# Performance work log

Measured on AMD Instinct MI355X. Metric: run time of the kernel, lower is better.

The kernel has to match this reference:

```python
import jax, jax.numpy as jnp
import numpy as np

EPS = 1e-06

def setup_inputs() -> dict:
    key = jax.random.key(0)
    k1, k2 = jax.random.split(key)
    x = jax.random.normal(k1, (8192, 4096), dtype=jnp.float32)
    # nn.Linear weight: [num_experts, input_dim]
    W = jax.random.normal(k2, (64, 4096), dtype=jnp.float32) * (1.0 / np.sqrt(4096.0))
    return {"x": x, "W": W}


def reference(x, W):
    # logits: [N, E]  (thin GEMM)
    logits = jnp.einsum('nd,ed->ne', x, W)
    gates = jax.nn.softmax(logits, axis=-1)
    # importance auxiliary loss: per-expert column sums, unbiased std (torch default)
    importance = gates.sum(axis=0)                      # [E]
    mean_imp = importance.mean()
    E = importance.shape[0]
    std_imp = jnp.sqrt(jnp.sum((importance - mean_imp) ** 2) / (E - 1))
    aux_loss = (std_imp / (mean_imp + EPS)) ** 2
    # top-k gates, renormalize with a second softmax
    top_k_gates, top_k_indices = jax.lax.top_k(gates, 2)  # [N, k]
    combine_weights = jax.nn.softmax(top_k_gates, axis=-1)
    return combine_weights, top_k_indices, aux_loss
```

## Files before the change

kernel.cpp:

```cpp
#include <hip/hip_runtime.h>
#include <math.h>

#define NROWS 8192
#define NK    4096
#define NE    64
#define NWV   8

typedef _Float16 f16x8 __attribute__((ext_vector_type(8)));
typedef float    f32x4 __attribute__((ext_vector_type(4)));

#define CVT8(H, L, V0, V1)                                            \
  do {                                                                \
    H[0] = (_Float16)V0.x; L[0] = (_Float16)(V0.x - (float)H[0]);     \
    H[1] = (_Float16)V0.y; L[1] = (_Float16)(V0.y - (float)H[1]);     \
    H[2] = (_Float16)V0.z; L[2] = (_Float16)(V0.z - (float)H[2]);     \
    H[3] = (_Float16)V0.w; L[3] = (_Float16)(V0.w - (float)H[3]);     \
    H[4] = (_Float16)V1.x; L[4] = (_Float16)(V1.x - (float)H[4]);     \
    H[5] = (_Float16)V1.y; L[5] = (_Float16)(V1.y - (float)H[5]);     \
    H[6] = (_Float16)V1.z; L[6] = (_Float16)(V1.z - (float)H[6]);     \
    H[7] = (_Float16)V1.w; L[7] = (_Float16)(V1.w - (float)H[7]);     \
  } while (0)

__global__ __launch_bounds__(256) void k_prep(const float* __restrict__ W,
                                              _Float16* __restrict__ Whi,
                                              _Float16* __restrict__ Wlo,
                                              float* __restrict__ imp) {
  const int idx = blockIdx.x * 256 + threadIdx.x;
  if (idx < NE) imp[idx] = 0.f;
  const int j    = idx & 7;
  const int lane = (idx >> 3) & 63;
  const int nt   = (idx >> 9) & 3;
  const int ksg  = idx >> 11;
  const int e = nt * 16 + (lane & 15);
  const int k = ksg * 32 + (lane >> 4) * 8 + j;
  const float w = W[(size_t)e * NK + k];
  const _Float16 wh = (_Float16)w;
  const _Float16 wl = (_Float16)(w - (float)wh);
  Whi[idx] = wh;
  Wlo[idx] = wl;
}

__global__ __launch_bounds__(512)
__attribute__((amdgpu_waves_per_eu(2, 2)))
void k_fused(const float* __restrict__ x,
             const _Float16* __restrict__ Whi,
             const _Float16* __restrict__ Wlo,
             float* __restrict__ out,
             float* __restrict__ imp) {
  __shared__ float plds[NWV][32][64];
  __shared__ float logit[32][64];
  __shared__ float simp[NWV][64];

  const int tid  = threadIdx.x;
  const int lane = tid & 63;
  const int wv   = __builtin_amdgcn_readfirstlane(tid >> 6);
  const int l15  = lane & 15;
  const int lhi  = lane >> 4;
  const int rbase = blockIdx.x * 32;
  const int k0    = wv * 512;

  const float* __restrict__ xp0 = x + (size_t)(rbase + l15) * NK + k0 + lhi * 8;
  const float* __restrict__ xp1 = xp0 + (size_t)16 * NK;
  const _Float16* __restrict__ whp = Whi + ((size_t)(wv * 16 * 4) * 64 + lane) * 8;
  const _Float16* __restrict__ wlp = Wlo + ((size_t)(wv * 16 * 4) * 64 + lane) * 8;

  f32x4 acc0[4], acc1[4];
#pragma unroll
  for (int nt = 0; nt < 4; ++nt) {
    acc0[nt] = (f32x4){0.f, 0.f, 0.f, 0.f};
    acc1[nt] = (f32x4){0.f, 0.f, 0.f, 0.f};
  }

  float4 ca0 = *(const float4*)(xp0);
  float4 ca1 = *(const float4*)(xp0 + 4);
  float4 cb0 = *(const float4*)(xp1);
  float4 cb1 = *(const float4*)(xp1 + 4);
  float4 na0 = *(const float4*)(xp0 + 32);
  float4 na1 = *(const float4*)(xp0 + 36);
  float4 nb0 = *(const float4*)(xp1 + 32);
  float4 nb1 = *(const float4*)(xp1 + 36);
  f16x8 whc[4], wlc[4], whn[4], wln[4];
#pragma unroll
  for (int nt = 0; nt < 4; ++nt) {
    whc[nt] = *(const f16x8*)(whp + nt * 512);
    wlc[nt] = *(const f16x8*)(wlp + nt * 512);
  }

#pragma unroll
  for (int ks = 0; ks < 16; ++ks) {
    if (ks < 15) {
      const size_t nb_ = (size_t)(ks + 1) * 2048;
#pragma unroll
      for (int nt = 0; nt < 4; ++nt) {
        whn[nt] = *(const f16x8*)(whp + nb_ + nt * 512);
        wln[nt] = *(const f16x8*)(wlp + nb_ + nt * 512);
      }
    }
    float4 pa0, pa1, pb0, pb1;
    if (ks + 2 < 16) {
      pa0 = *(const float4*)(xp0 + (ks + 2) * 32);
      pa1 = *(const float4*)(xp0 + (ks + 2) * 32 + 4);
      pb0 = *(const float4*)(xp1 + (ks + 2) * 32);
      pb1 = *(const float4*)(xp1 + (ks + 2) * 32 + 4);
    }

    f16x8 ah, al, bh, bl;
    CVT8(ah, al, ca0, ca1);
    CVT8(bh, bl, cb0, cb1);

#pragma unroll
    for (int nt = 0; nt < 4; ++nt) {
      acc0[nt] = __builtin_amdgcn_mfma_f32_16x16x32_f16(ah, whc[nt], acc0[nt], 0, 0, 0);
      acc1[nt] = __builtin_amdgcn_mfma_f32_16x16x32_f16(bh, whc[nt], acc1[nt], 0, 0, 0);
    }
#pragma unroll
    for (int nt = 0; nt < 4; ++nt) {
      acc0[nt] = __builtin_amdgcn_mfma_f32_16x16x32_f16(ah, wlc[nt], acc0[nt], 0, 0, 0);
      acc1[nt] = __builtin_amdgcn_mfma_f32_16x16x32_f16(bh, wlc[nt], acc1[nt], 0, 0, 0);
    }
#pragma unroll
    for (int nt = 0; nt < 4; ++nt) {
      acc0[nt] = __builtin_amdgcn_mfma_f32_16x16x32_f16(al, whc[nt], acc0[nt], 0, 0, 0);
      acc1[nt] = __builtin_amdgcn_mfma_f32_16x16x32_f16(bl, whc[nt], acc1[nt], 0, 0, 0);
    }

    ca0 = na0; ca1 = na1; cb0 = nb0; cb1 = nb1;
    na0 = pa0; na1 = pa1; nb0 = pb0; nb1 = pb1;
#pragma unroll
    for (int nt = 0; nt < 4; ++nt) { whc[nt] = whn[nt]; wlc[nt] = wln[nt]; }
  }

#pragma unroll
  for (int nt = 0; nt < 4; ++nt)
#pragma unroll
    for (int r = 0; r < 4; ++r) {
      plds[wv][lhi * 4 + r][nt * 16 + l15]      = acc0[nt][r];
      plds[wv][16 + lhi * 4 + r][nt * 16 + l15] = acc1[nt][r];
    }
  __syncthreads();

#pragma unroll
  for (int i = 0; i < 4; ++i) {
    const int elem = tid + i * 512;
    const int row  = elem >> 6;
    const int col  = elem & 63;
    const float s01 = plds[0][row][col] + plds[1][row][col];
    const float s23 = plds[2][row][col] + plds[3][row][col];
    const float s45 = plds[4][row][col] + plds[5][row][col];
    const float s67 = plds[6][row][col] + plds[7][row][col];
    logit[row][col] = ((s01 + s23) + (s45 + s67));
  }
  __syncthreads();

  float impacc = 0.f;
#pragma unroll 1
  for (int i = 0; i < 4; ++i) {
    const int rl  = wv * 4 + i;
    const int row = rbase + rl;
    const float lg = logit[rl][lane];

    float m = lg;
#pragma unroll
    for (int d = 1; d < 64; d <<= 1) m = fmaxf(m, __shfl_xor(m, d));
    float p = expf(lg - m);
    float s = p;
#pragma unroll
    for (int d = 1; d < 64; d <<= 1) s += __shfl_xor(s, d);
    const float gate = p / s;
    impacc += gate;

    const unsigned long long key =
        ((unsigned long long)__float_as_uint(gate) << 32) | (unsigned)(63 - lane);
    unsigned long long k1 = key;
#pragma unroll
    for (int d = 1; d < 64; d <<= 1) {
      unsigned long long o = __shfl_xor(k1, d);
      if (o > k1) k1 = o;
    }
    const int e1 = 63 - (int)(k1 & 63ull);
    unsigned long long k2 = (lane == e1) ? 0ull : key;
#pragma unroll
    for (int d = 1; d < 64; d <<= 1) {
      unsigned long long o = __shfl_xor(k2, d);
      if (o > k2) k2 = o;
    }
    const int e2 = 63 - (int)(k2 & 63ull);

    if (lane == 0) {
      const float g1 = __uint_as_float((unsigned)(k1 >> 32));
      const float g2 = __uint_as_float((unsigned)(k2 >> 32));
      const float tt  = expf(g2 - g1);
      const float inv = 1.f / (1.f + tt);
      out[(size_t)row * 2]     = inv;
      out[(size_t)row * 2 + 1] = tt * inv;
      out[(size_t)NROWS * 2 + row * 2]     = (float)e1;
      out[(size_t)NROWS * 2 + row * 2 + 1] = (float)e2;
    }
  }
  simp[wv][lane] = impacc;
  __syncthreads();

  if (tid < NE) {
    const float v = (((simp[0][tid] + simp[1][tid]) + (simp[2][tid] + simp[3][tid])) +
                     ((simp[4][tid] + simp[5][tid]) + (simp[6][tid] + simp[7][tid])));
    atomicAdd(&imp[tid], v);
  }
}

__global__ void k_aux(const float* __restrict__ imp, float* __restrict__ out) {
  const int lane = threadIdx.x;
  const float v = imp[lane];
  float s = v;
#pragma unroll
  for (int d = 1; d < 64; d <<= 1) s += __shfl_xor(s, d);
  const float mean = s / 64.f;
  const float dv = v - mean;
  float sq = dv * dv;
#pragma unroll
  for (int d = 1; d < 64; d <<= 1) sq += __shfl_xor(sq, d);
  const float stdv = sqrtf(sq / 63.f);
  const float r = stdv / (mean + 1e-6f);
  if (lane == 0) out[(size_t)NROWS * 4] = r * r;
}

extern "C" void kernel_launch(void* const* d_in, const int* in_sizes, int n_in,
                              void* d_out, int out_size, void* d_ws, size_t ws_size,
                              hipStream_t stream) {
  const float* x = (const float*)d_in[0];
  const float* W = (const float*)d_in[1];
  float* out  = (float*)d_out;
  _Float16* Whi = (_Float16*)d_ws;
  _Float16* Wlo = Whi + (size_t)NE * NK;
  float* imp  = (float*)(Wlo + (size_t)NE * NK);

  hipLaunchKernelGGL(k_prep,  dim3(1024), dim3(256), 0, stream, W, Whi, Wlo, imp);
  hipLaunchKernelGGL(k_fused, dim3(256),  dim3(512), 0, stream, x, Whi, Wlo, out, imp);
  hipLaunchKernelGGL(k_aux,   dim3(1),    dim3(64),  0, stream, imp, out);
}
```

Baseline: 47.89 us.

## Stage x through LDS with async global_load_lds triple buffering and M/N wave split

```diff
diff --git a/kernel.cpp b/kernel.cpp
--- a/kernel.cpp
+++ b/kernel.cpp
@@ -4,7 +4,6 @@
 #define NROWS 8192
 #define NK    4096
 #define NE    64
-#define NWV   8
 
 typedef _Float16 f16x8 __attribute__((ext_vector_type(8)));
 typedef float    f32x4 __attribute__((ext_vector_type(4)));
@@ -20,6 +19,12 @@
     H[6] = (_Float16)V1.z; L[6] = (_Float16)(V1.z - (float)H[6]);     \
     H[7] = (_Float16)V1.w; L[7] = (_Float16)(V1.w - (float)H[7]);     \
   } while (0)
+
+__device__ __forceinline__ void gload16(const void* g, void* l) {
+  __builtin_amdgcn_global_load_lds(
+      (const __attribute__((address_space(1))) unsigned int*)g,
+      (__attribute__((address_space(3))) unsigned int*)l, 16, 0, 0);
+}
 
 __global__ __launch_bounds__(256) void k_prep(const float* __restrict__ W,
                                               _Float16* __restrict__ Whi,
@@ -40,116 +45,81 @@
   Wlo[idx] = wl;
 }
 
-__global__ __launch_bounds__(512)
-__attribute__((amdgpu_waves_per_eu(2, 2)))
-void k_fused(const float* __restrict__ x,
-             const _Float16* __restrict__ Whi,
-             const _Float16* __restrict__ Wlo,
-             float* __restrict__ out,
-             float* __restrict__ imp) {
-  __shared__ float plds[NWV][32][64];
-  __shared__ float logit[32][64];
-  __shared__ float simp[NWV][64];
+#define STAGE(cc)                                                             \
+  if (wv < 6) {                                                               \
+    _Pragma("unroll")                                                         \
+    for (int jj = 0; jj < 3; ++jj) {                                          \
+      const int j  = wv * 3 + jj;                       \
+      const int t  = j * 64 + lane;                     \
+      const int rr = t / 9;                             \
+      const int u  = t - rr * 9;                        \
+      const int ksl_ = rr >> 5, r_ = rr & 31;                                 \
+      const int uu = (u < 8) ? u : 7;             \
+      const float* gsrc = x + (size_t)(rbase + r_) * NK +                     \
+                          ((cc) * 128 + ksl_ * 32 + uu * 4);                  \
+      gload16(gsrc, (char*)&X[(cc) % 3][0][0][0] + j * 1024);                 \
+    }                                                                         \
+  }
+
+__global__ __launch_bounds__(512) void k_fused(const float* __restrict__ x,
+                                               const _Float16* __restrict__ Whi,
+                                               const _Float16* __restrict__ Wlo,
+                                               float* __restrict__ out,
+                                               float* __restrict__ imp) {
+  __shared__ float X[3][4][32][36];
 
   const int tid  = threadIdx.x;
   const int lane = tid & 63;
   const int wv   = __builtin_amdgcn_readfirstlane(tid >> 6);
+  const int mi   = wv >> 2;
+  const int ni   = wv & 3;
   const int l15  = lane & 15;
   const int lhi  = lane >> 4;
   const int rbase = blockIdx.x * 32;
-  const int k0    = wv * 512;
-
-  const float* __restrict__ xp0 = x + (size_t)(rbase + l15) * NK + k0 + lhi * 8;
-  const float* __restrict__ xp1 = xp0 + (size_t)16 * NK;
-  const _Float16* __restrict__ whp = Whi + ((size_t)(wv * 16 * 4) * 64 + lane) * 8;
-  const _Float16* __restrict__ wlp = Wlo + ((size_t)(wv * 16 * 4) * 64 + lane) * 8;
-
-  f32x4 acc0[4], acc1[4];
-#pragma unroll
-  for (int nt = 0; nt < 4; ++nt) {
-    acc0[nt] = (f32x4){0.f, 0.f, 0.f, 0.f};
-    acc1[nt] = (f32x4){0.f, 0.f, 0.f, 0.f};
-  }
-
-  float4 ca0 = *(const float4*)(xp0);
-  float4 ca1 = *(const float4*)(xp0 + 4);
-  float4 cb0 = *(const float4*)(xp1);
-  float4 cb1 = *(const float4*)(xp1 + 4);
-  float4 na0 = *(const float4*)(xp0 + 32);
-  float4 na1 = *(const float4*)(xp0 + 36);
-  float4 nb0 = *(const float4*)(xp1 + 32);
-  float4 nb1 = *(const float4*)(xp1 + 36);
-  f16x8 whc[4], wlc[4], whn[4], wln[4];
-#pragma unroll
-  for (int nt = 0; nt < 4; ++nt) {
-    whc[nt] = *(const f16x8*)(whp + nt * 512);
-    wlc[nt] = *(const f16x8*)(wlp + nt * 512);
-  }
-
-#pragma unroll
-  for (int ks = 0; ks < 16; ++ks) {
-    if (ks < 15) {
-      const size_t nb_ = (size_t)(ks + 1) * 2048;
-#pragma unroll
-      for (int nt = 0; nt < 4; ++nt) {
-        whn[nt] = *(const f16x8*)(whp + nb_ + nt * 512);
-        wln[nt] = *(const f16x8*)(wlp + nb_ + nt * 512);
-      }
-    }
-    float4 pa0, pa1, pb0, pb1;
-    if (ks + 2 < 16) {
-      pa0 = *(const float4*)(xp0 + (ks + 2) * 32);
-      pa1 = *(const float4*)(xp0 + (ks + 2) * 32 + 4);
-      pb0 = *(const float4*)(xp1 + (ks + 2) * 32);
-      pb1 = *(const float4*)(xp1 + (ks + 2) * 32 + 4);
-    }
-
-    f16x8 ah, al, bh, bl;
-    CVT8(ah, al, ca0, ca1);
-    CVT8(bh, bl, cb0, cb1);
-
-#pragma unroll
-    for (int nt = 0; nt < 4; ++nt) {
-      acc0[nt] = __builtin_amdgcn_mfma_f32_16x16x32_f16(ah, whc[nt], acc0[nt], 0, 0, 0);
-      acc1[nt] = __builtin_amdgcn_mfma_f32_16x16x32_f16(bh, whc[nt], acc1[nt], 0, 0, 0);
-    }
-#pragma unroll
-    for (int nt = 0; nt < 4; ++nt) {
-      acc0[nt] = __builtin_amdgcn_mfma_f32_16x16x32_f16(ah, wlc[nt], acc0[nt], 0, 0, 0);
-      acc1[nt] = __builtin_amdgcn_mfma_f32_16x16x32_f16(bh, wlc[nt], acc1[nt], 0, 0, 0);
-    }
-#pragma unroll
-    for (int nt = 0; nt < 4; ++nt) {
-      acc0[nt] = __builtin_amdgcn_mfma_f32_16x16x32_f16(al, whc[nt], acc0[nt], 0, 0, 0);
-      acc1[nt] = __builtin_amdgcn_mfma_f32_16x16x32_f16(bl, whc[nt], acc1[nt], 0, 0, 0);
-    }
-
-    ca0 = na0; ca1 = na1; cb0 = nb0; cb1 = nb1;
-    na0 = pa0; na1 = pa1; nb0 = pb0; nb1 = pb1;
-#pragma unroll
-    for (int nt = 0; nt < 4; ++nt) { whc[nt] = whn[nt]; wlc[nt] = wln[nt]; }
-  }
-
-#pragma unroll
-  for (int nt = 0; nt < 4; ++nt)
-#pragma unroll
-    for (int r = 0; r < 4; ++r) {
-      plds[wv][lhi * 4 + r][nt * 16 + l15]      = acc0[nt][r];
-      plds[wv][16 + lhi * 4 + r][nt * 16 + l15] = acc1[nt][r];
-    }
-  __syncthreads();
-
-#pragma unroll
-  for (int i = 0; i < 4; ++i) {
-    const int elem = tid + i * 512;
-    const int row  = elem >> 6;
-    const int col  = elem & 63;
-    const float s01 = plds[0][row][col] + plds[1][row][col];
-    const float s23 = plds[2][row][col] + plds[3][row][col];
-    const float s45 = plds[4][row][col] + plds[5][row][col];
-    const float s67 = plds[6][row][col] + plds[7][row][col];
-    logit[row][col] = ((s01 + s23) + (s45 + s67));
-  }
+  const int mrow  = mi * 16 + l15;
+
+  STAGE(0);
+  STAGE(1);
+  __syncthreads();
+
+  f32x4 accp = (f32x4){0.f, 0.f, 0.f, 0.f};
+  f32x4 accq = (f32x4){0.f, 0.f, 0.f, 0.f};
+
+#pragma unroll 1
+  for (int c = 0; c < 32; ++c) {
+    f16x8 wh[4], wl[4];
+#pragma unroll
+    for (int ksl = 0; ksl < 4; ++ksl) {
+      const size_t fo = (((size_t)(c * 4 + ksl) * 4 + ni) * 64 + lane) * 8;
+      wh[ksl] = *(const f16x8*)(Whi + fo);
+      wl[ksl] = *(const f16x8*)(Wlo + fo);
+    }
+    if (c + 2 < 32) { STAGE(c + 2); }
+
+    const float (*Xc)[32][36] = X[c % 3];
+#pragma unroll
+    for (int ksl = 0; ksl < 4; ++ksl) {
+      const float4 xa = *(const float4*)&Xc[ksl][mrow][lhi * 8];
+      const float4 xb = *(const float4*)&Xc[ksl][mrow][lhi * 8 + 4];
+      f16x8 ah, al;
+      CVT8(ah, al, xa, xb);
+      accp = __builtin_amdgcn_mfma_f32_16x16x32_f16(ah, wh[ksl], accp, 0, 0, 0);
+      accq = __builtin_amdgcn_mfma_f32_16x16x32_f16(ah, wl[ksl], accq, 0, 0, 0);
+      accq = __builtin_amdgcn_mfma_f32_16x16x32_f16(al, wh[ksl], accq, 0, 0, 0);
+    }
+
+    __builtin_amdgcn_s_barrier();
+    __builtin_amdgcn_sched_barrier(0);
+  }
+
+  __syncthreads();
+  float* logitp = &X[0][0][0][0];
+  float* simpp  = logitp + 32 * 64;
+
+  const f32x4 accf = accp + accq;
+#pragma unroll
+  for (int r = 0; r < 4; ++r)
+    logitp[(mi * 16 + lhi * 4 + r) * 64 + ni * 16 + l15] = accf[r];
   __syncthreads();
 
   float impacc = 0.f;
@@ -157,7 +127,7 @@
   for (int i = 0; i < 4; ++i) {
     const int rl  = wv * 4 + i;
     const int row = rbase + rl;
-    const float lg = logit[rl][lane];
+    const float lg = logitp[rl * 64 + lane];
 
     float m = lg;
 #pragma unroll
@@ -197,12 +167,15 @@
       out[(size_t)NROWS * 2 + row * 2 + 1] = (float)e2;
     }
   }
-  simp[wv][lane] = impacc;
+  simpp[wv * 64 + lane] = impacc;
   __syncthreads();
 
   if (tid < NE) {
-    const float v = (((simp[0][tid] + simp[1][tid]) + (simp[2][tid] + simp[3][tid])) +
-                     ((simp[4][tid] + simp[5][tid]) + (simp[6][tid] + simp[7][tid])));
+    const float v =
+        (((simpp[0 * 64 + tid] + simpp[1 * 64 + tid]) +
+          (simpp[2 * 64 + tid] + simpp[3 * 64 + tid])) +
+         ((simpp[4 * 64 + tid] + simpp[5 * 64 + tid]) +
+          (simpp[6 * 64 + tid] + simpp[7 * 64 + tid])));
     atomicAdd(&imp[tid], v);
   }
 }
```

Measured after the change: 71.07 us. 48.4% more time.

## Split K across blocks, stage W in LDS, finish softmax in separate kernel

Applied to the files above, without the earlier changes.

```diff
diff --git a/kernel.cpp b/kernel.cpp
--- a/kernel.cpp
+++ b/kernel.cpp
@@ -4,7 +4,7 @@
 #define NROWS 8192
 #define NK    4096
 #define NE    64
-#define NWV   8
+#define NSEG  8
 
 typedef _Float16 f16x8 __attribute__((ext_vector_type(8)));
 typedef float    f32x4 __attribute__((ext_vector_type(4)));
@@ -21,55 +21,33 @@
     H[7] = (_Float16)V1.w; L[7] = (_Float16)(V1.w - (float)H[7]);     \
   } while (0)
 
-__global__ __launch_bounds__(256) void k_prep(const float* __restrict__ W,
-                                              _Float16* __restrict__ Whi,
-                                              _Float16* __restrict__ Wlo,
-                                              float* __restrict__ imp) {
-  const int idx = blockIdx.x * 256 + threadIdx.x;
-  if (idx < NE) imp[idx] = 0.f;
-  const int j    = idx & 7;
-  const int lane = (idx >> 3) & 63;
-  const int nt   = (idx >> 9) & 3;
-  const int ksg  = idx >> 11;
-  const int e = nt * 16 + (lane & 15);
-  const int k = ksg * 32 + (lane >> 4) * 8 + j;
-  const float w = W[(size_t)e * NK + k];
-  const _Float16 wh = (_Float16)w;
-  const _Float16 wl = (_Float16)(w - (float)wh);
-  Whi[idx] = wh;
-  Wlo[idx] = wl;
-}
-
 __global__ __launch_bounds__(512)
 __attribute__((amdgpu_waves_per_eu(2, 2)))
-void k_fused(const float* __restrict__ x,
-             const _Float16* __restrict__ Whi,
-             const _Float16* __restrict__ Wlo,
-             float* __restrict__ out,
-             float* __restrict__ imp) {
-  __shared__ float plds[NWV][32][64];
-  __shared__ float logit[32][64];
-  __shared__ float simp[NWV][64];
+void k_main(const float* __restrict__ x,
+            const float* __restrict__ W,
+            float* __restrict__ part,
+            float* __restrict__ imp,
+            unsigned* __restrict__ cnt) {
+  __shared__ f16x8 WH[16][4][64];
+  __shared__ f16x8 WL[16][4][64];
 
   const int tid  = threadIdx.x;
   const int lane = tid & 63;
   const int wv   = __builtin_amdgcn_readfirstlane(tid >> 6);
+  const int rg   = blockIdx.x >> 3;
+  const int seg  = blockIdx.x & 7;
   const int l15  = lane & 15;
   const int lhi  = lane >> 4;
-  const int rbase = blockIdx.x * 32;
-  const int k0    = wv * 512;
+  const int rbase = rg * 256 + wv * 32;
+  const int k0    = seg * 512;
+
+  if (blockIdx.x == 0) {
+    if (tid < NE) imp[tid] = 0.f;
+    if (tid == NE) *cnt = 0u;
+  }
 
   const float* __restrict__ xp0 = x + (size_t)(rbase + l15) * NK + k0 + lhi * 8;
   const float* __restrict__ xp1 = xp0 + (size_t)16 * NK;
-  const _Float16* __restrict__ whp = Whi + ((size_t)(wv * 16 * 4) * 64 + lane) * 8;
-  const _Float16* __restrict__ wlp = Wlo + ((size_t)(wv * 16 * 4) * 64 + lane) * 8;
-
-  f32x4 acc0[4], acc1[4];
-#pragma unroll
-  for (int nt = 0; nt < 4; ++nt) {
-    acc0[nt] = (f32x4){0.f, 0.f, 0.f, 0.f};
-    acc1[nt] = (f32x4){0.f, 0.f, 0.f, 0.f};
-  }
 
   float4 ca0 = *(const float4*)(xp0);
   float4 ca1 = *(const float4*)(xp0 + 4);
@@ -79,23 +57,34 @@
   float4 na1 = *(const float4*)(xp0 + 36);
   float4 nb0 = *(const float4*)(xp1 + 32);
   float4 nb1 = *(const float4*)(xp1 + 36);
-  f16x8 whc[4], wlc[4], whn[4], wln[4];
+
+  {
+    const int nt   = wv & 3;
+    const int half = wv >> 2;
+    const int e  = nt * 16 + l15;
+    const float* __restrict__ wrow = W + (size_t)e * NK + k0 + lhi * 8;
+#pragma unroll
+    for (int g = 0; g < 8; ++g) {
+      const int gk = half * 8 + g;
+      const float4 w0 = *(const float4*)(wrow + gk * 32);
+      const float4 w1 = *(const float4*)(wrow + gk * 32 + 4);
+      f16x8 hi, lo;
+      CVT8(hi, lo, w0, w1);
+      WH[gk][nt][lane] = hi;
+      WL[gk][nt][lane] = lo;
+    }
+  }
+  __syncthreads();
+
+  f32x4 acc0[4], acc1[4];
 #pragma unroll
   for (int nt = 0; nt < 4; ++nt) {
-    whc[nt] = *(const f16x8*)(whp + nt * 512);
-    wlc[nt] = *(const f16x8*)(wlp + nt * 512);
+    acc0[nt] = (f32x4){0.f, 0.f, 0.f, 0.f};
+    acc1[nt] = (f32x4){0.f, 0.f, 0.f, 0.f};
   }
 
 #pragma unroll
   for (int ks = 0; ks < 16; ++ks) {
-    if (ks < 15) {
-      const size_t nb_ = (size_t)(ks + 1) * 2048;
-#pragma unroll
-      for (int nt = 0; nt < 4; ++nt) {
-        whn[nt] = *(const f16x8*)(whp + nb_ + nt * 512);
-        wln[nt] = *(const f16x8*)(wlp + nb_ + nt * 512);
-      }
-    }
     float4 pa0, pa1, pb0, pb1;
     if (ks + 2 < 16) {
       pa0 = *(const float4*)(xp0 + (ks + 2) * 32);
@@ -103,6 +92,12 @@
       pb0 = *(const float4*)(xp1 + (ks + 2) * 32);
       pb1 = *(const float4*)(xp1 + (ks + 2) * 32 + 4);
     }
+    f16x8 wh[4], wl[4];
+#pragma unroll
+    for (int nt = 0; nt < 4; ++nt) {
+      wh[nt] = WH[ks][nt][lane];
+      wl[nt] = WL[ks][nt][lane];
+    }
 
     f16x8 ah, al, bh, bl;
     CVT8(ah, al, ca0, ca1);
@@ -110,54 +105,55 @@
 
 #pragma unroll
     for (int nt = 0; nt < 4; ++nt) {
-      acc0[nt] = __builtin_amdgcn_mfma_f32_16x16x32_f16(ah, whc[nt], acc0[nt], 0, 0, 0);
-      acc1[nt] = __builtin_amdgcn_mfma_f32_16x16x32_f16(bh, whc[nt], acc1[nt], 0, 0, 0);
-    }
-#pragma unroll
-    for (int nt = 0; nt < 4; ++nt) {
-      acc0[nt] = __builtin_amdgcn_mfma_f32_16x16x32_f16(ah, wlc[nt], acc0[nt], 0, 0, 0);
-      acc1[nt] = __builtin_amdgcn_mfma_f32_16x16x32_f16(bh, wlc[nt], acc1[nt], 0, 0, 0);
-    }
-#pragma unroll
-    for (int nt = 0; nt < 4; ++nt) {
-      acc0[nt] = __builtin_amdgcn_mfma_f32_16x16x32_f16(al, whc[nt], acc0[nt], 0, 0, 0);
-      acc1[nt] = __builtin_amdgcn_mfma_f32_16x16x32_f16(bl, whc[nt], acc1[nt], 0, 0, 0);
+      acc0[nt] = __builtin_amdgcn_mfma_f32_16x16x32_f16(ah, wh[nt], acc0[nt], 0, 0, 0);
+      acc1[nt] = __builtin_amdgcn_mfma_f32_16x16x32_f16(bh, wh[nt], acc1[nt], 0, 0, 0);
+    }
+#pragma unroll
+    for (int nt = 0; nt < 4; ++nt) {
+      acc0[nt] = __builtin_amdgcn_mfma_f32_16x16x32_f16(ah, wl[nt], acc0[nt], 0, 0, 0);
+      acc1[nt] = __builtin_amdgcn_mfma_f32_16x16x32_f16(bh, wl[nt], acc1[nt], 0, 0, 0);
+    }
+#pragma unroll
+    for (int nt = 0; nt < 4; ++nt) {
+      acc0[nt] = __builtin_amdgcn_mfma_f32_16x16x32_f16(al, wh[nt], acc0[nt], 0, 0, 0);
+      acc1[nt] = __builtin_amdgcn_mfma_f32_16x16x32_f16(bl, wh[nt], acc1[nt], 0, 0, 0);
     }
 
     ca0 = na0; ca1 = na1; cb0 = nb0; cb1 = nb1;
     na0 = pa0; na1 = pa1; nb0 = pb0; nb1 = pb1;
-#pragma unroll
-    for (int nt = 0; nt < 4; ++nt) { whc[nt] = whn[nt]; wlc[nt] = wln[nt]; }
-  }
-
+  }
+
+  float* dst0 = part + ((size_t)seg * NROWS + rbase) * NE;
+  float* dst1 = dst0 + (size_t)16 * NE;
 #pragma unroll
   for (int nt = 0; nt < 4; ++nt)
 #pragma unroll
     for (int r = 0; r < 4; ++r) {
-      plds[wv][lhi * 4 + r][nt * 16 + l15]      = acc0[nt][r];
-      plds[wv][16 + lhi * 4 + r][nt * 16 + l15] = acc1[nt][r];
-    }
-  __syncthreads();
-
-#pragma unroll
-  for (int i = 0; i < 4; ++i) {
-    const int elem = tid + i * 512;
-    const int row  = elem >> 6;
-    const int col  = elem & 63;
-    const float s01 = plds[0][row][col] + plds[1][row][col];
-    const float s23 = plds[2][row][col] + plds[3][row][col];
-    const float s45 = plds[4][row][col] + plds[5][row][col];
-    const float s67 = plds[6][row][col] + plds[7][row][col];
-    logit[row][col] = ((s01 + s23) + (s45 + s67));
-  }
-  __syncthreads();
-
+      dst0[(size_t)(lhi * 4 + r) * NE + nt * 16 + l15] = acc0[nt][r];
+      dst1[(size_t)(lhi * 4 + r) * NE + nt * 16 + l15] = acc1[nt][r];
+    }
+}
+
+__global__ __launch_bounds__(256) void k_soft(const float* __restrict__ part,
+                                              float* __restrict__ out,
+                                              float* __restrict__ imp,
+                                              unsigned* __restrict__ cnt) {
+  __shared__ float simp[4][64];
+  __shared__ int lastflag;
+  const int tid  = threadIdx.x;
+  const int lane = tid & 63;
+  const int wv   = tid >> 6;
+  const int rbase = blockIdx.x * 32 + wv * 8;
   float impacc = 0.f;
-#pragma unroll 1
-  for (int i = 0; i < 4; ++i) {
-    const int rl  = wv * 4 + i;
-    const int row = rbase + rl;
-    const float lg = logit[rl][lane];
+
+  for (int i = 0; i < 8; ++i) {
+    const int row = rbase + i;
+    float v[NSEG];
+#pragma unroll
+    for (int s = 0; s < NSEG; ++s)
+      v[s] = part[((size_t)s * NROWS + row) * NE + lane];
+    const float lg = (((v[0] + v[1]) + (v[2] + v[3])) +
+                      ((v[4] + v[5]) + (v[6] + v[7])));
 
     float m = lg;
 #pragma unroll
@@ -197,30 +193,35 @@
       out[(size_t)NROWS * 2 + row * 2 + 1] = (float)e2;
     }
   }
+
   simp[wv][lane] = impacc;
   __syncthreads();
-
   if (tid < NE) {
-    const float v = (((simp[0][tid] + simp[1][tid]) + (simp[2][tid] + simp[3][tid])) +
-                     ((simp[4][tid] + simp[5][tid]) + (simp[6][tid] + simp[7][tid])));
+    const float v = simp[0][tid] + simp[1][tid] + simp[2][tid] + simp[3][tid];
     atomicAdd(&imp[tid], v);
   }
-}
-
-__global__ void k_aux(const float* __restrict__ imp, float* __restrict__ out) {
-  const int lane = threadIdx.x;
-  const float v = imp[lane];
-  float s = v;
-#pragma unroll
-  for (int d = 1; d < 64; d <<= 1) s += __shfl_xor(s, d);
-  const float mean = s / 64.f;
-  const float dv = v - mean;
-  float sq = dv * dv;
-#pragma unroll
-  for (int d = 1; d < 64; d <<= 1) sq += __shfl_xor(sq, d);
-  const float stdv = sqrtf(sq / 63.f);
-  const float r = stdv / (mean + 1e-6f);
-  if (lane == 0) out[(size_t)NROWS * 4] = r * r;
+  __syncthreads();
+
+  if (tid == 0) {
+    const unsigned old = atomicAdd(cnt, 1u);
+    lastflag = (old == 255u) ? 1 : 0;
+  }
+  __syncthreads();
+
+  if (lastflag && tid < NE) {
+    const float v = atomicAdd(&imp[tid], 0.f);
+    float s = v;
+#pragma unroll
+    for (int d = 1; d < 64; d <<= 1) s += __shfl_xor(s, d);
+    const float mean = s / 64.f;
+    const float dv = v - mean;
+    float sq = dv * dv;
+#pragma unroll
+    for (int d = 1; d < 64; d <<= 1) sq += __shfl_xor(sq, d);
+    const float stdv = sqrtf(sq / 63.f);
+    const float r = stdv / (mean + 1e-6f);
+    if (tid == 0) out[(size_t)NROWS * 4] = r * r;
+  }
 }
 
 extern "C" void kernel_launch(void* const* d_in, const int* in_sizes, int n_in,
@@ -229,11 +230,10 @@
   const float* x = (const float*)d_in[0];
   const float* W = (const float*)d_in[1];
   float* out  = (float*)d_out;
-  _Float16* Whi = (_Float16*)d_ws;
-  _Float16* Wlo = Whi + (size_t)NE * NK;
-  float* imp  = (float*)(Wlo + (size_t)NE * NK);
-
-  hipLaunchKernelGGL(k_prep,  dim3(1024), dim3(256), 0, stream, W, Whi, Wlo, imp);
-  hipLaunchKernelGGL(k_fused, dim3(256),  dim3(512), 0, stream, x, Whi, Wlo, out, imp);
-  hipLaunchKernelGGL(k_aux,   dim3(1),    dim3(64),  0, stream, imp, out);
+  float* part = (float*)d_ws;
+  float* imp  = part + (size_t)NSEG * NROWS * NE;
+  unsigned* cnt = (unsigned*)(imp + NE);
+
+  hipLaunchKernelGGL(k_main, dim3(256), dim3(512), 0, stream, x, W, part, imp, cnt);
+  hipLaunchKernelGGL(k_soft, dim3(256), dim3(256), 0, stream, part, out, imp, cnt);
 }
```

Result: slower. 53.84 us (+12.4%).
